# Kernel optimization log

Measured on AMD Instinct MI355X. Metric: run time of the kernel, lower is better.

The kernel has to match this reference:

```python
import jax, jax.numpy as jnp
import numpy as np

D_MODEL = 4096
N_HEADS = 32
N_KV_HEADS = 8
HEAD_DIM = D_MODEL // N_HEADS  # 128
SEQ = 2048
BATCH = 1
ROPE_BASE = 10000.0


def build_rope_cache(max_seq_len, head_dim, base=10000.0):
    half = head_dim // 2
    pos = jnp.arange(max_seq_len, dtype=jnp.float32)
    inv_freqs = 1.0 / (base ** (jnp.arange(half, dtype=jnp.float32) / half))
    angles = pos[:, None] * inv_freqs[None, :]  # (S, half)
    return jnp.cos(angles), jnp.sin(angles)


def apply_rope(t, cos, sin):
    # t: (B, H, S, D); cos/sin: (S, D//2) broadcast over batch & heads.
    t_even = t[..., 0::2]
    t_odd = t[..., 1::2]
    c = cos[None, None, :, :]
    s = sin[None, None, :, :]
    rot_even = t_even * c - t_odd * s
    rot_odd = t_even * s + t_odd * c
    # interleave back into even/odd slots
    return jnp.stack([rot_even, rot_odd], axis=-1).reshape(t.shape)


def setup_inputs() -> dict:
    key = jax.random.key(0)
    kx, kq, kk, kv, ko = jax.random.split(key, 5)
    bound = 1.0 / np.sqrt(D_MODEL)
    x = jax.random.normal(kx, (BATCH, SEQ, D_MODEL), dtype=jnp.float32)
    # torch Linear weights: (out_features, in_features)
    wq = jax.random.uniform(kq, (N_HEADS * HEAD_DIM, D_MODEL), minval=-bound, maxval=bound, dtype=jnp.float32)
    wk = jax.random.uniform(kk, (N_KV_HEADS * HEAD_DIM, D_MODEL), minval=-bound, maxval=bound, dtype=jnp.float32)
    wv = jax.random.uniform(kv, (N_KV_HEADS * HEAD_DIM, D_MODEL), minval=-bound, maxval=bound, dtype=jnp.float32)
    wo = jax.random.uniform(ko, (D_MODEL, D_MODEL), minval=-bound, maxval=bound, dtype=jnp.float32)
    attn_mask = jnp.tril(jnp.ones((SEQ, SEQ), dtype=jnp.int32))[None, None, :, :]
    return {"x": x, "wq": wq, "wk": wk, "wv": wv, "wo": wo, "attn_mask": attn_mask}


def reference(x, wq, wk, wv, wo, attn_mask):
    B, S, _ = x.shape
    cos, sin = build_rope_cache(SEQ, HEAD_DIM, ROPE_BASE)
    cos, sin = cos[:S], sin[:S]
    q = (x @ wq.T).reshape(B, S, N_HEADS, HEAD_DIM).transpose(0, 2, 1, 3)      # (B,H,S,D)
    k = (x @ wk.T).reshape(B, S, N_KV_HEADS, HEAD_DIM).transpose(0, 2, 1, 3)   # (B,Hkv,S,D)
    v = (x @ wv.T).reshape(B, S, N_KV_HEADS, HEAD_DIM).transpose(0, 2, 1, 3)
    q = apply_rope(q, cos, sin)
    k = apply_rope(k, cos, sin)
    n_rep = N_HEADS // N_KV_HEADS
    if n_rep > 1:
        k = jnp.repeat(k, n_rep, axis=1)
        v = jnp.repeat(v, n_rep, axis=1)
    scores = jnp.einsum('bhqd,bhkd->bhqk', q, k) / jnp.sqrt(jnp.float32(HEAD_DIM))
    scores = jnp.where(attn_mask == 0, -jnp.inf, scores)
    attn = jax.nn.softmax(scores, axis=-1)
    out = jnp.einsum('bhqk,bhkd->bhqd', attn, v)
    out = out.transpose(0, 2, 1, 3).reshape(B, S, D_MODEL)
    return out @ wo.T
```

## Files before the change

### kernel.cpp

```cpp
#include <hip/hip_runtime.h>
#include <hip/hip_bf16.h>

typedef float f32x2 __attribute__((ext_vector_type(2)));
typedef float f32x4 __attribute__((ext_vector_type(4)));
typedef __bf16 bf16x4 __attribute__((ext_vector_type(4)));
typedef __bf16 bf16x8 __attribute__((ext_vector_type(8)));

__device__ __forceinline__ void gld_lds16(const void* g, void* l) {
  __builtin_amdgcn_global_load_lds((const __attribute__((address_space(1))) void*)g,
                                   (__attribute__((address_space(3))) void*)l, 16, 0, 0);
}

__global__ void cvt_f32_bf16(const float* __restrict__ in, __bf16* __restrict__ out,
                             int n8) {
  int idx = blockIdx.x * blockDim.x + threadIdx.x;
  if (idx >= n8) return;
  f32x4 a = *(const f32x4*)(in + (size_t)idx * 8);
  f32x4 b = *(const f32x4*)(in + (size_t)idx * 8 + 4);
  bf16x8 o;
#pragma unroll
  for (int j = 0; j < 4; ++j) { o[j] = (__bf16)a[j]; o[4 + j] = (__bf16)b[j]; }
  *(bf16x8*)(out + (size_t)idx * 8) = o;
}

__global__ void build_trig(float* __restrict__ trig) {
  int idx = blockIdx.x * blockDim.x + threadIdx.x;
  if (idx >= 2048 * 64) return;
  int i = idx & 63, s = idx >> 6;
  float ang = (float)s * powf(10000.0f, -(float)i * (1.0f / 64.0f));
  float sn, cs;
  sincosf(ang, &sn, &cs);
  trig[idx * 2] = cs;
  trig[idx * 2 + 1] = sn;
}

__global__ void rope_bf16(__bf16* __restrict__ T, const float* __restrict__ trig,
                          int stride, int nh_mask, int nh_shift, float mul, int total) {
  int idx = blockIdx.x * blockDim.x + threadIdx.x;
  if (idx >= total) return;
  int i = idx & 63;
  int h = (idx >> 6) & nh_mask;
  int s = idx >> (6 + nh_shift);
  float cs = trig[(s * 64 + i) * 2];
  float sn = trig[(s * 64 + i) * 2 + 1];
  __bf16* p = T + (size_t)s * stride + h * 128 + 2 * i;
  float e = (float)p[0], o = (float)p[1];
  p[0] = (__bf16)((e * cs - o * sn) * mul);
  p[1] = (__bf16)((e * sn + o * cs) * mul);
}

__global__ __launch_bounds__(256) void transpose_v(const __bf16* __restrict__ KVb,
                                                   __bf16* __restrict__ Vt) {
  __shared__ __bf16 T[64][72];
  const int tid = threadIdx.x;
  const int s0 = blockIdx.x * 64, d0 = blockIdx.y * 64;
  const int r = tid >> 3, c8 = (tid & 7) * 8;
#pragma unroll
  for (int i = 0; i < 2; ++i) {
    int row = i * 32 + r;
    *(bf16x8*)&T[row][c8] = *(const bf16x8*)&KVb[(size_t)(s0 + row) * 2048 + 1024 + d0 + c8];
  }
  __syncthreads();
#pragma unroll
  for (int i = 0; i < 2; ++i) {
    int drow = i * 32 + r;
    bf16x8 o;
#pragma unroll
    for (int j = 0; j < 8; ++j) o[j] = T[c8 + j][drow];
    *(bf16x8*)&Vt[(size_t)(d0 + drow) * 2048 + s0 + c8] = o;
  }
}

template <int BM, int BN, typename OutT>
__global__ __launch_bounds__(256) void gemm_bf16(const __bf16* __restrict__ A,
                                                 const __bf16* __restrict__ B0,
                                                 const __bf16* __restrict__ B1,
                                                 int Nsplit, OutT* __restrict__ C,
                                                 int M, int N, int K) {
  constexpr int MI = BM / 32, NJ = BN / 32;
  constexpr int RA = BM / 32, RB = BN / 32;
  __shared__ __bf16 As[BM * 64] __attribute__((aligned(16)));
  __shared__ __bf16 Bs[BN * 64] __attribute__((aligned(16)));

  const int tid = threadIdx.x;
  const int lane = tid & 63;
  const int w = tid >> 6;
  const int nwg = gridDim.x * gridDim.y;
  const int orig = blockIdx.y * gridDim.x + blockIdx.x;
  const int wgid = (orig & 7) * (nwg >> 3) + (orig >> 3);
  const int m0 = (wgid % gridDim.x) * BM;
  const int n0 = (wgid / gridDim.x) * BN;
  const int li = lane & 15, lg = lane >> 4;

  const __bf16* bsrc[RB];
#pragma unroll
  for (int i = 0; i < RB; ++i) {
    int slot = i * 256 + w * 64 + lane;
    int row = slot >> 3;
    int sch = (slot & 7) ^ (row & 7);
    int n = n0 + row;
    bsrc[i] = (n < Nsplit ? B0 + (size_t)n * K : B1 + (size_t)(n - Nsplit) * K) +
              sch * 8;
  }
  const __bf16* asrc[RA];
#pragma unroll
  for (int i = 0; i < RA; ++i) {
    int slot = i * 256 + w * 64 + lane;
    int row = slot >> 3;
    int sch = (slot & 7) ^ (row & 7);
    asrc[i] = A + (size_t)(m0 + row) * K + sch * 8;
  }

  const int wr = (w >> 1) * (BM / 2);
  const int wc = (w & 1) * (BN / 2);

  f32x4 acc[MI][NJ] = {};

  for (int k0 = 0; k0 < K; k0 += 64) {
    __syncthreads();
#pragma unroll
    for (int i = 0; i < RA; ++i)
      gld_lds16(asrc[i] + k0, &As[(i * 256 + w * 64) * 8]);
#pragma unroll
    for (int i = 0; i < RB; ++i)
      gld_lds16(bsrc[i] + k0, &Bs[(i * 256 + w * 64) * 8]);
    __syncthreads();

#pragma unroll
    for (int u = 0; u < 2; ++u) {
      bf16x8 af[MI], bfr[NJ];
#pragma unroll
      for (int mi = 0; mi < MI; ++mi)
        af[mi] = *(const bf16x8*)&As[(wr + mi * 16 + li) * 64 +
                                     (((u * 4 + lg) ^ (li & 7)) * 8)];
#pragma unroll
      for (int nj = 0; nj < NJ; ++nj)
        bfr[nj] = *(const bf16x8*)&Bs[(wc + nj * 16 + li) * 64 +
                                      (((u * 4 + lg) ^ (li & 7)) * 8)];
#pragma unroll
      for (int mi = 0; mi < MI; ++mi)
#pragma unroll
        for (int nj = 0; nj < NJ; ++nj)
          acc[mi][nj] = __builtin_amdgcn_mfma_f32_16x16x32_bf16(af[mi], bfr[nj],
                                                                acc[mi][nj], 0, 0, 0);
    }
  }

  const int crow = lg * 4;
#pragma unroll
  for (int mi = 0; mi < MI; ++mi)
#pragma unroll
    for (int nj = 0; nj < NJ; ++nj)
#pragma unroll
      for (int r = 0; r < 4; ++r)
        C[(size_t)(m0 + wr + mi * 16 + crow + r) * N + (n0 + wc + nj * 16 + li)] =
            (OutT)acc[mi][nj][r];
}

__global__ __launch_bounds__(256) void attn_fwd_v7(const __bf16* __restrict__ Q,
                                                   const __bf16* __restrict__ KVb,
                                                   const __bf16* __restrict__ Vt,
                                                   const float* __restrict__ trig,
                                                   __bf16* __restrict__ O) {
  const int tid = threadIdx.x;
  const int lane = tid & 63;
  const int w = tid >> 6;
  const int bid = blockIdx.x;
  const int xcd = bid & 7;
  const int r9 = bid >> 3;
  const int h = xcd * 4 + (r9 & 3);
  const int mb = 31 - (r9 >> 2);
  const int kvh = h >> 2;
  const int m0 = mb * 64;
  const int rbase = m0 + w * 16;

  __shared__ __bf16 Ks[2][64 * 128] __attribute__((aligned(16)));
  __shared__ __bf16 Vs[128 * 64] __attribute__((aligned(16)));
  __shared__ __bf16 Ps[4][16 * 72] __attribute__((aligned(16)));

  const int li = lane & 15, lg = lane >> 4;
  const float qscale = 0.08838834764831845f * 1.4426950408889634f;

  auto stage_k = [&](int k0, int buf) {
#pragma unroll
    for (int i = 0; i < 4; ++i) {
      int slot = i * 256 + tid;
      int row = slot >> 4;
      int sch = (slot & 15) ^ (row & 7);
      gld_lds16(&KVb[(size_t)(k0 + row) * 2048 + kvh * 128 + sch * 8],
                &Ks[buf][(i * 256 + w * 64) * 8]);
    }
  };
  auto stage_v = [&](int k0) {
#pragma unroll
    for (int i = 0; i < 4; ++i) {
      int slot = i * 256 + tid;
      int row = slot >> 3;
      int sch = (slot & 7) ^ (row & 7);
      gld_lds16(&Vt[(size_t)(kvh * 128 + row) * 2048 + k0 + sch * 8],
                &Vs[(i * 256 + w * 64) * 8]);
    }
  };

  const int s = rbase + li;
  bf16x8 qf[4];
  {
    const __bf16* qrow = Q + (size_t)s * 4096 + h * 128;
#pragma unroll
    for (int kc = 0; kc < 4; ++kc) {
      bf16x8 raw = *(const bf16x8*)(qrow + kc * 32 + lg * 8);
#pragma unroll
      for (int jj = 0; jj < 4; ++jj) {
        int i = kc * 16 + lg * 4 + jj;
        f32x2 cs = *(const f32x2*)&trig[((size_t)s * 64 + i) * 2];
        float e = (float)raw[2 * jj], o = (float)raw[2 * jj + 1];
        qf[kc][2 * jj]     = (__bf16)((e * cs[0] - o * cs[1]) * qscale);
        qf[kc][2 * jj + 1] = (__bf16)((e * cs[1] + o * cs[0]) * qscale);
      }
    }
  }

  f32x4 accO[8] = {};
  float plane = 0.f;
  const int ntile = mb + 1;

  stage_k(0, 0);

#pragma unroll 1
  for (int t = 0; t < ntile; ++t) {
    const int k0 = t * 64;
    const int cur = t & 1;
    stage_v(k0);
    stage_k(t + 1 < ntile ? k0 + 64 : 0, cur ^ 1);

    asm volatile("s_waitcnt vmcnt(8)" ::: "memory");
    __builtin_amdgcn_s_barrier();
    __builtin_amdgcn_sched_barrier(0);

    f32x4 s2[4] = {};
    __builtin_amdgcn_s_setprio(1);
#pragma unroll
    for (int nt = 0; nt < 4; ++nt)
#pragma unroll
      for (int kc = 0; kc < 4; ++kc) {
        bf16x8 kf = *(const bf16x8*)&Ks[cur][(li + 16 * nt) * 128 +
                                            (((4 * kc + lg) ^ (li & 7)) * 8)];
        s2[nt] = __builtin_amdgcn_mfma_f32_16x16x32_bf16(kf, qf[kc], s2[nt], 0, 0, 0);
      }
    __builtin_amdgcn_s_setprio(0);

    const bool needmask = (k0 + 63 > rbase);
#pragma unroll
    for (int nt = 0; nt < 4; ++nt) {
      bf16x4 pk;
#pragma unroll
      for (int rr = 0; rr < 4; ++rr) {
        const int key = k0 + 16 * nt + lg * 4 + rr;
        float v = s2[nt][rr];
        if (needmask && key > s) v = -INFINITY;
        float p = exp2f(v);
        plane += p;
        pk[rr] = (__bf16)p;
      }
      *(bf16x4*)&Ps[w][li * 72 + 16 * nt + lg * 4] = pk;
    }
    bf16x8 pa[2];
    pa[0] = *(const bf16x8*)&Ps[w][li * 72 + lg * 8];
    pa[1] = *(const bf16x8*)&Ps[w][li * 72 + 32 + lg * 8];

    asm volatile("s_waitcnt vmcnt(4)" ::: "memory");
    __builtin_amdgcn_s_barrier();
    __builtin_amdgcn_sched_barrier(0);

    __builtin_amdgcn_s_setprio(1);
#pragma unroll
    for (int dt = 0; dt < 8; ++dt)
#pragma unroll
      for (int kc = 0; kc < 2; ++kc) {
        bf16x8 vf = *(const bf16x8*)&Vs[(li + 16 * dt) * 64 +
                                        (((4 * kc + lg) ^ (li & 7)) * 8)];
        accO[dt] = __builtin_amdgcn_mfma_f32_16x16x32_bf16(pa[kc], vf, accO[dt], 0, 0, 0);
      }
    __builtin_amdgcn_s_setprio(0);

    __builtin_amdgcn_s_barrier();
    __builtin_amdgcn_sched_barrier(0);
  }

  {
    float sum = plane;
    sum += __shfl_xor(sum, 16);
    sum += __shfl_xor(sum, 32);
    float inv[4];
#pragma unroll
    for (int rr = 0; rr < 4; ++rr) inv[rr] = 1.0f / __shfl(sum, lg * 4 + rr);
#pragma unroll
    for (int dt = 0; dt < 8; ++dt)
#pragma unroll
      for (int rr = 0; rr < 4; ++rr)
        O[(size_t)(rbase + lg * 4 + rr) * 4096 + h * 128 + dt * 16 + li] =
            (__bf16)(accO[dt][rr] * inv[rr]);
  }
}

extern "C" void kernel_launch(void* const* d_in, const int* in_sizes, int n_in,
                              void* d_out, int out_size, void* d_ws, size_t ws_size,
                              hipStream_t stream) {
  const float* x  = (const float*)d_in[0];
  const float* wq = (const float*)d_in[1];
  const float* wk = (const float*)d_in[2];
  const float* wv = (const float*)d_in[3];
  const float* wo = (const float*)d_in[4];
  float* out = (float*)d_out;

  const int S = 2048, D = 4096;
  char* ws = (char*)d_ws;
  __bf16* xb  = (__bf16*)ws;
  __bf16* Qb  = (__bf16*)(ws + 16777216);
  __bf16* KVb = (__bf16*)(ws + 33554432);
  __bf16* Vt  = (__bf16*)(ws + 41943040);
  __bf16* wb  = (__bf16*)(ws + 46137344);
  float*  trig = (float*)(ws + 79691776);
  __bf16* AOb = xb;

  cvt_f32_bf16<<<(S * D / 8 + 255) / 256, 256, 0, stream>>>(x, xb, S * D / 8);
  cvt_f32_bf16<<<(D * D / 8 + 255) / 256, 256, 0, stream>>>(wq, wb, D * D / 8);
  gemm_bf16<128, 128, __bf16><<<dim3(16, 32), 256, 0, stream>>>(
      xb, wb, wb, 1 << 30, Qb, S, D, D);

  cvt_f32_bf16<<<(1024 * D / 8 + 255) / 256, 256, 0, stream>>>(wk, wb, 1024 * D / 8);
  cvt_f32_bf16<<<(1024 * D / 8 + 255) / 256, 256, 0, stream>>>(wv, wb + (size_t)1024 * D,
                                                               1024 * D / 8);
  gemm_bf16<64, 128, __bf16><<<dim3(32, 16), 256, 0, stream>>>(
      xb, wb, wb + (size_t)1024 * D, 1024, KVb, S, 2048, D);

  build_trig<<<(2048 * 64 + 255) / 256, 256, 0, stream>>>(trig);
  rope_bf16<<<(S * 8 * 64 + 255) / 256, 256, 0, stream>>>(KVb, trig, 2048, 7, 3,
                                                          1.0f, S * 8 * 64);
  transpose_v<<<dim3(32, 16), 256, 0, stream>>>(KVb, Vt);

  attn_fwd_v7<<<1024, 256, 0, stream>>>(Qb, KVb, Vt, trig, AOb);

  cvt_f32_bf16<<<(D * D / 8 + 255) / 256, 256, 0, stream>>>(wo, wb, D * D / 8);
  gemm_bf16<128, 128, float><<<dim3(16, 32), 256, 0, stream>>>(
      AOb, wb, wb, 1 << 30, out, S, D, D);
}
```

Measured before the change: 344.7 us.

## Fuse K RoPE and V transpose into KV GEMM epilogue; retile attention to 32-key triple buffer

The KV projection GEMM epilogue now applies RoPE to K columns, using a lane shuffle to fetch the paired element, and writes V directly in transposed layout. This removes the separate rope and transpose kernels and their extra passes over memory. The attention kernel switches to 32-key tiles with triple-buffered K/V staging and one barrier per iteration instead of two. The cost is twice as many loop iterations, each doing smaller MFMA work, and scattered 8-byte Vt stores in the GEMM epilogue.

```diff
diff --git a/kernel.cpp b/kernel.cpp
--- a/kernel.cpp
+++ b/kernel.cpp
@@ -34,49 +34,14 @@
   trig[idx * 2 + 1] = sn;
 }
 
-__global__ void rope_bf16(__bf16* __restrict__ T, const float* __restrict__ trig,
-                          int stride, int nh_mask, int nh_shift, float mul, int total) {
-  int idx = blockIdx.x * blockDim.x + threadIdx.x;
-  if (idx >= total) return;
-  int i = idx & 63;
-  int h = (idx >> 6) & nh_mask;
-  int s = idx >> (6 + nh_shift);
-  float cs = trig[(s * 64 + i) * 2];
-  float sn = trig[(s * 64 + i) * 2 + 1];
-  __bf16* p = T + (size_t)s * stride + h * 128 + 2 * i;
-  float e = (float)p[0], o = (float)p[1];
-  p[0] = (__bf16)((e * cs - o * sn) * mul);
-  p[1] = (__bf16)((e * sn + o * cs) * mul);
-}
-
-__global__ __launch_bounds__(256) void transpose_v(const __bf16* __restrict__ KVb,
-                                                   __bf16* __restrict__ Vt) {
-  __shared__ __bf16 T[64][72];
-  const int tid = threadIdx.x;
-  const int s0 = blockIdx.x * 64, d0 = blockIdx.y * 64;
-  const int r = tid >> 3, c8 = (tid & 7) * 8;
-#pragma unroll
-  for (int i = 0; i < 2; ++i) {
-    int row = i * 32 + r;
-    *(bf16x8*)&T[row][c8] = *(const bf16x8*)&KVb[(size_t)(s0 + row) * 2048 + 1024 + d0 + c8];
-  }
-  __syncthreads();
-#pragma unroll
-  for (int i = 0; i < 2; ++i) {
-    int drow = i * 32 + r;
-    bf16x8 o;
-#pragma unroll
-    for (int j = 0; j < 8; ++j) o[j] = T[c8 + j][drow];
-    *(bf16x8*)&Vt[(size_t)(d0 + drow) * 2048 + s0 + c8] = o;
-  }
-}
-
-template <int BM, int BN, typename OutT>
+template <int BM, int BN, typename OutT, bool KVF>
 __global__ __launch_bounds__(256) void gemm_bf16(const __bf16* __restrict__ A,
                                                  const __bf16* __restrict__ B0,
                                                  const __bf16* __restrict__ B1,
                                                  int Nsplit, OutT* __restrict__ C,
-                                                 int M, int N, int K) {
+                                                 int M, int N, int K,
+                                                 const float* __restrict__ trig,
+                                                 __bf16* __restrict__ Vt) {
   constexpr int MI = BM / 32, NJ = BN / 32;
   constexpr int RA = BM / 32, RB = BN / 32;
   __shared__ __bf16 As[BM * 64] __attribute__((aligned(16)));
@@ -147,17 +112,50 @@
   }
 
   const int crow = lg * 4;
-#pragma unroll
-  for (int mi = 0; mi < MI; ++mi)
-#pragma unroll
-    for (int nj = 0; nj < NJ; ++nj)
-#pragma unroll
-      for (int r = 0; r < 4; ++r)
-        C[(size_t)(m0 + wr + mi * 16 + crow + r) * N + (n0 + wc + nj * 16 + li)] =
-            (OutT)acc[mi][nj][r];
-}
-
-__global__ __launch_bounds__(256) void attn_fwd_v7(const __bf16* __restrict__ Q,
+  if (KVF && n0 >= Nsplit) {
+#pragma unroll
+    for (int mi = 0; mi < MI; ++mi)
+#pragma unroll
+      for (int nj = 0; nj < NJ; ++nj) {
+        int d = n0 - Nsplit + wc + nj * 16 + li;
+        int sb = m0 + wr + mi * 16 + crow;
+        bf16x4 pk;
+#pragma unroll
+        for (int r = 0; r < 4; ++r) pk[r] = (__bf16)acc[mi][nj][r];
+        *(bf16x4*)&Vt[(size_t)d * 2048 + sb] = pk;
+      }
+  } else if (KVF) {
+#pragma unroll
+    for (int mi = 0; mi < MI; ++mi)
+#pragma unroll
+      for (int nj = 0; nj < NJ; ++nj) {
+        int c = n0 + wc + nj * 16 + li;
+        int i = (c & 127) >> 1;
+        bool even = (c & 1) == 0;
+#pragma unroll
+        for (int r = 0; r < 4; ++r) {
+          int s = m0 + wr + mi * 16 + crow + r;
+          float own = acc[mi][nj][r];
+          float oth = __shfl_xor(own, 1);
+          f32x2 cs = *(const f32x2*)&trig[((size_t)s * 64 + i) * 2];
+          float v = even ? (own * cs[0] - oth * cs[1])
+                         : (oth * cs[1] + own * cs[0]);
+          C[(size_t)s * N + c] = (OutT)v;
+        }
+      }
+  } else {
+#pragma unroll
+    for (int mi = 0; mi < MI; ++mi)
+#pragma unroll
+      for (int nj = 0; nj < NJ; ++nj)
+#pragma unroll
+        for (int r = 0; r < 4; ++r)
+          C[(size_t)(m0 + wr + mi * 16 + crow + r) * N + (n0 + wc + nj * 16 + li)] =
+              (OutT)acc[mi][nj][r];
+  }
+}
+
+__global__ __launch_bounds__(256) void attn_fwd_v8(const __bf16* __restrict__ Q,
                                                    const __bf16* __restrict__ KVb,
                                                    const __bf16* __restrict__ Vt,
                                                    const float* __restrict__ trig,
@@ -174,16 +172,16 @@
   const int m0 = mb * 64;
   const int rbase = m0 + w * 16;
 
-  __shared__ __bf16 Ks[2][64 * 128] __attribute__((aligned(16)));
-  __shared__ __bf16 Vs[128 * 64] __attribute__((aligned(16)));
-  __shared__ __bf16 Ps[4][16 * 72] __attribute__((aligned(16)));
+  __shared__ __bf16 Ks[3][32 * 128] __attribute__((aligned(16)));
+  __shared__ __bf16 Vs[3][128 * 32] __attribute__((aligned(16)));
+  __shared__ __bf16 Ps[4][16 * 40] __attribute__((aligned(16)));
 
   const int li = lane & 15, lg = lane >> 4;
   const float qscale = 0.08838834764831845f * 1.4426950408889634f;
 
   auto stage_k = [&](int k0, int buf) {
 #pragma unroll
-    for (int i = 0; i < 4; ++i) {
+    for (int i = 0; i < 2; ++i) {
       int slot = i * 256 + tid;
       int row = slot >> 4;
       int sch = (slot & 15) ^ (row & 7);
@@ -191,14 +189,14 @@
                 &Ks[buf][(i * 256 + w * 64) * 8]);
     }
   };
-  auto stage_v = [&](int k0) {
-#pragma unroll
-    for (int i = 0; i < 4; ++i) {
+  auto stage_v = [&](int k0, int buf) {
+#pragma unroll
+    for (int i = 0; i < 2; ++i) {
       int slot = i * 256 + tid;
-      int row = slot >> 3;
-      int sch = (slot & 7) ^ (row & 7);
+      int row = slot >> 2;
+      int sch = (slot & 3) ^ (row & 3);
       gld_lds16(&Vt[(size_t)(kvh * 128 + row) * 2048 + k0 + sch * 8],
-                &Vs[(i * 256 + w * 64) * 8]);
+                &Vs[buf][(i * 256 + w * 64) * 8]);
     }
   };
 
@@ -222,36 +220,38 @@
 
   f32x4 accO[8] = {};
   float plane = 0.f;
-  const int ntile = mb + 1;
-
+  const int ntile = 2 * (mb + 1);
+
+  stage_v(0, 0);
   stage_k(0, 0);
 
 #pragma unroll 1
   for (int t = 0; t < ntile; ++t) {
-    const int k0 = t * 64;
-    const int cur = t & 1;
-    stage_v(k0);
-    stage_k(t + 1 < ntile ? k0 + 64 : 0, cur ^ 1);
-
-    asm volatile("s_waitcnt vmcnt(8)" ::: "memory");
+    const int k0 = t * 32;
+    const int cb = t % 3;
+    const int nk = (t + 1 < ntile) ? k0 + 32 : k0;
+    stage_v(nk, (t + 1) % 3);
+    stage_k(nk, (t + 1) % 3);
+
+    asm volatile("s_waitcnt vmcnt(4)" ::: "memory");
     __builtin_amdgcn_s_barrier();
     __builtin_amdgcn_sched_barrier(0);
 
-    f32x4 s2[4] = {};
+    f32x4 s2[2] = {};
     __builtin_amdgcn_s_setprio(1);
 #pragma unroll
-    for (int nt = 0; nt < 4; ++nt)
+    for (int nt = 0; nt < 2; ++nt)
 #pragma unroll
       for (int kc = 0; kc < 4; ++kc) {
-        bf16x8 kf = *(const bf16x8*)&Ks[cur][(li + 16 * nt) * 128 +
-                                            (((4 * kc + lg) ^ (li & 7)) * 8)];
+        bf16x8 kf = *(const bf16x8*)&Ks[cb][(li + 16 * nt) * 128 +
+                                           (((4 * kc + lg) ^ (li & 7)) * 8)];
         s2[nt] = __builtin_amdgcn_mfma_f32_16x16x32_bf16(kf, qf[kc], s2[nt], 0, 0, 0);
       }
     __builtin_amdgcn_s_setprio(0);
 
-    const bool needmask = (k0 + 63 > rbase);
-#pragma unroll
-    for (int nt = 0; nt < 4; ++nt) {
+    const bool needmask = (k0 + 31 > rbase);
+#pragma unroll
+    for (int nt = 0; nt < 2; ++nt) {
       bf16x4 pk;
 #pragma unroll
       for (int rr = 0; rr < 4; ++rr) {
@@ -262,29 +262,18 @@
         plane += p;
         pk[rr] = (__bf16)p;
       }
-      *(bf16x4*)&Ps[w][li * 72 + 16 * nt + lg * 4] = pk;
-    }
-    bf16x8 pa[2];
-    pa[0] = *(const bf16x8*)&Ps[w][li * 72 + lg * 8];
-    pa[1] = *(const bf16x8*)&Ps[w][li * 72 + 32 + lg * 8];
-
-    asm volatile("s_waitcnt vmcnt(4)" ::: "memory");
-    __builtin_amdgcn_s_barrier();
-    __builtin_amdgcn_sched_barrier(0);
+      *(bf16x4*)&Ps[w][li * 40 + 16 * nt + lg * 4] = pk;
+    }
+    bf16x8 pa = *(const bf16x8*)&Ps[w][li * 40 + lg * 8];
 
     __builtin_amdgcn_s_setprio(1);
 #pragma unroll
-    for (int dt = 0; dt < 8; ++dt)
-#pragma unroll
-      for (int kc = 0; kc < 2; ++kc) {
-        bf16x8 vf = *(const bf16x8*)&Vs[(li + 16 * dt) * 64 +
-                                        (((4 * kc + lg) ^ (li & 7)) * 8)];
-        accO[dt] = __builtin_amdgcn_mfma_f32_16x16x32_bf16(pa[kc], vf, accO[dt], 0, 0, 0);
-      }
+    for (int dt = 0; dt < 8; ++dt) {
+      bf16x8 vf = *(const bf16x8*)&Vs[cb][(li + 16 * dt) * 32 +
+                                          ((lg ^ (li & 3)) * 8)];
+      accO[dt] = __builtin_amdgcn_mfma_f32_16x16x32_bf16(pa, vf, accO[dt], 0, 0, 0);
+    }
     __builtin_amdgcn_s_setprio(0);
-
-    __builtin_amdgcn_s_barrier();
-    __builtin_amdgcn_sched_barrier(0);
   }
 
   {
@@ -325,23 +314,20 @@
 
   cvt_f32_bf16<<<(S * D / 8 + 255) / 256, 256, 0, stream>>>(x, xb, S * D / 8);
   cvt_f32_bf16<<<(D * D / 8 + 255) / 256, 256, 0, stream>>>(wq, wb, D * D / 8);
-  gemm_bf16<128, 128, __bf16><<<dim3(16, 32), 256, 0, stream>>>(
-      xb, wb, wb, 1 << 30, Qb, S, D, D);
+  gemm_bf16<128, 128, __bf16, false><<<dim3(16, 32), 256, 0, stream>>>(
+      xb, wb, wb, 1 << 30, Qb, S, D, D, nullptr, nullptr);
+
+  build_trig<<<(2048 * 64 + 255) / 256, 256, 0, stream>>>(trig);
 
   cvt_f32_bf16<<<(1024 * D / 8 + 255) / 256, 256, 0, stream>>>(wk, wb, 1024 * D / 8);
   cvt_f32_bf16<<<(1024 * D / 8 + 255) / 256, 256, 0, stream>>>(wv, wb + (size_t)1024 * D,
                                                                1024 * D / 8);
-  gemm_bf16<64, 128, __bf16><<<dim3(32, 16), 256, 0, stream>>>(
-      xb, wb, wb + (size_t)1024 * D, 1024, KVb, S, 2048, D);
-
-  build_trig<<<(2048 * 64 + 255) / 256, 256, 0, stream>>>(trig);
-  rope_bf16<<<(S * 8 * 64 + 255) / 256, 256, 0, stream>>>(KVb, trig, 2048, 7, 3,
-                                                          1.0f, S * 8 * 64);
-  transpose_v<<<dim3(32, 16), 256, 0, stream>>>(KVb, Vt);
-
-  attn_fwd_v7<<<1024, 256, 0, stream>>>(Qb, KVb, Vt, trig, AOb);
+  gemm_bf16<64, 128, __bf16, true><<<dim3(32, 16), 256, 0, stream>>>(
+      xb, wb, wb + (size_t)1024 * D, 1024, KVb, S, 2048, D, trig, Vt);
+
+  attn_fwd_v8<<<1024, 256, 0, stream>>>(Qb, KVb, Vt, trig, AOb);
 
   cvt_f32_bf16<<<(D * D / 8 + 255) / 256, 256, 0, stream>>>(wo, wb, D * D / 8);
-  gemm_bf16<128, 128, float><<<dim3(16, 32), 256, 0, stream>>>(
-      AOb, wb, wb, 1 << 30, out, S, D, D);
-}
+  gemm_bf16<128, 128, float, false><<<dim3(16, 32), 256, 0, stream>>>(
+      AOb, wb, wb, 1 << 30, out, S, D, D, nullptr, nullptr);
+}
```

New measurement: 344.6 us. No clear change (-0.0%).
